# Optimization experiments

Measured on AMD Instinct MI355X. Metric: run time of the kernel, lower is better.

Reference implementation:

```python
import jax, jax.numpy as jnp
import numpy as np

ALPHA = 0.25
GAMMA = 2.0
MARGIN = 1.0
LAMBDA_GRAPH = 0.1
N = 8192
D = 128


def setup_inputs() -> dict:
    key = jax.random.key(0)
    k1, k2, k3, k4 = jax.random.split(key, 4)
    preds = jax.random.normal(k1, (N,), dtype=jnp.float32)
    targets = jax.random.randint(k2, (N,), 0, 2).astype(jnp.float32)  # binary labels
    features = jax.random.normal(k3, (N, D), dtype=jnp.float32)
    graph_features = jax.random.normal(k4, (N, D), dtype=jnp.float32)
    return {"preds": preds, "targets": targets, "features": features,
            "graph_features": graph_features}


def _focal_loss(preds, targets):
    # numerically stable BCE-with-logits, reduction='none'
    bce = jnp.maximum(preds, 0.0) - preds * targets + jnp.log1p(jnp.exp(-jnp.abs(preds)))
    pt = jnp.exp(-bce)
    return jnp.mean(ALPHA * (1.0 - pt) ** GAMMA * bce)


def _contrastive_loss(features, labels):
    # squared pairwise distances via ||a||^2 + ||b||^2 - 2 a.b  -> [N, N]
    sqn = jnp.sum(features * features, axis=-1)
    sq = sqn[:, None] + sqn[None, :] - 2.0 * (features @ features.T)
    sq = jnp.maximum(sq, 0.0)
    # safe sqrt (gradient-safe at 0)
    pos = sq > 0.0
    dist = jnp.where(pos, jnp.sqrt(jnp.where(pos, sq, 1.0)), 0.0)
    same = labels[:, None] == labels[None, :]
    # same-label pairs: dist^2 == sq ; different: clamp(margin - dist, 0)^2
    per_pair = jnp.where(same, sq, jnp.maximum(MARGIN - dist, 0.0) ** 2)
    return jnp.mean(per_pair)  # sum / N^2


def _graph_reg_loss(graph_features):
    diff = graph_features[1:] - graph_features[:-1]
    return jnp.mean(jnp.sqrt(jnp.sum(diff * diff, axis=1)))


def reference(preds, targets, features, graph_features):
    return (_focal_loss(preds, targets)
            + _contrastive_loss(features, targets)
            + LAMBDA_GRAPH * _graph_reg_loss(graph_features))
```

## Files before the change

### kernel.cpp

```cpp
#include <hip/hip_runtime.h>
#include <hip/hip_bf16.h>


#define N_PTS 8192
#define DIM 128

typedef __bf16 bf16x8 __attribute__((ext_vector_type(8)));
typedef float f32x4 __attribute__((ext_vector_type(4)));

#define FBF_OFF   0
#define SQN_OFF   (N_PTS * DIM * 2)
#define CPART_OFF (SQN_OFF + N_PTS * 4)
#define FPART_OFF (CPART_OFF + 4096 * 4)
#define GPART_OFF (FPART_OFF + 32 * 4)

__global__ __launch_bounds__(256) void prep_kernel(const float* __restrict__ feat,
                                                   __bf16* __restrict__ fbf,
                                                   float* __restrict__ sqn) {
    const int w = threadIdx.x >> 6;
    const int lane = threadIdx.x & 63;
    const int r = blockIdx.x * 4 + w;
    const float2 v = *reinterpret_cast<const float2*>(feat + r * DIM + lane * 2);
    union { __bf16 h[2]; unsigned u; } pk;
    pk.h[0] = (__bf16)v.x; pk.h[1] = (__bf16)v.y;
    reinterpret_cast<unsigned*>(fbf)[r * (DIM / 2) + lane] = pk.u;
    float s = v.x * v.x + v.y * v.y;
    #pragma unroll
    for (int off = 32; off > 0; off >>= 1) s += __shfl_down(s, off);
    if (lane == 0) sqn[r] = s;
}

__global__ __launch_bounds__(256) void focal_kernel(const float* __restrict__ preds,
                                                    const float* __restrict__ targets,
                                                    float* __restrict__ f_part) {
    const int i = blockIdx.x * 256 + threadIdx.x;
    const float p = preds[i], t = targets[i];
    const float bce = fmaxf(p, 0.f) - p * t + log1pf(expf(-fabsf(p)));
    const float pt = expf(-bce);
    const float om = 1.f - pt;
    float v = 0.25f * om * om * bce;
    #pragma unroll
    for (int off = 32; off > 0; off >>= 1) v += __shfl_down(v, off);
    __shared__ float red[4];
    if ((threadIdx.x & 63) == 0) red[threadIdx.x >> 6] = v;
    __syncthreads();
    if (threadIdx.x == 0) f_part[blockIdx.x] = red[0] + red[1] + red[2] + red[3];
}

__global__ __launch_bounds__(256) void graph_kernel(const float* __restrict__ gf,
                                                    float* __restrict__ g_part) {
    const int w = threadIdx.x >> 6;
    const int lane = threadIdx.x & 63;
    float acc = 0.f;
    #pragma unroll
    for (int it = 0; it < 8; ++it) {
        const int r = blockIdx.x * 4 + w + it * 1024;
        if (r < N_PTS - 1) {
            const float2 a = *reinterpret_cast<const float2*>(gf + r * DIM + lane * 2);
            const float2 b = *reinterpret_cast<const float2*>(gf + (r + 1) * DIM + lane * 2);
            const float dx = b.x - a.x, dy = b.y - a.y;
            float s = dx * dx + dy * dy;
            #pragma unroll
            for (int off = 32; off > 0; off >>= 1) s += __shfl_down(s, off);
            if (lane == 0) acc += sqrtf(s);
        }
    }
    __shared__ float red[4];
    if (lane == 0) red[w] = acc;
    __syncthreads();
    if (threadIdx.x == 0) g_part[blockIdx.x] = red[0] + red[1] + red[2] + red[3];
}

__global__ __launch_bounds__(256) void pair_kernel(const __bf16* __restrict__ fbf,
                                                   const float* __restrict__ sqn,
                                                   const float* __restrict__ targets,
                                                   float* __restrict__ c_part) {
    const int bi = blockIdx.x, bj = blockIdx.y;
    const int bid = bj * 64 + bi;
    if (bj < bi) {
        if (threadIdx.x == 0) c_part[bid] = 0.f;
        return;
    }
    __shared__ __align__(16) char smem[65536];
    const int tid = threadIdx.x;
    const int lane = tid & 63;
    const int wv = tid >> 6;
    const int quad = lane >> 4;
    const int m15 = lane & 15;
    const int ibase = bi * 128, jbase = bj * 128;

    #pragma unroll
    for (int it = 0; it < 16; ++it) {
        const int p = it * 256 + tid;
        const int r = (p & 2047) >> 4;
        const int s = p & 15;
        const int c = s ^ (r & 15);
        const int grow = ((p >> 11) ? jbase : ibase) + r;
        const uint4 v = *reinterpret_cast<const uint4*>(
            reinterpret_cast<const char*>(fbf) + grow * 256 + c * 16);
        *reinterpret_cast<uint4*>(smem + p * 16) = v;
    }
    __syncthreads();

    const int wm = wv >> 1, wn = wv & 1;
    f32x4 acc[4][4];
    #pragma unroll
    for (int a = 0; a < 4; ++a)
        #pragma unroll
        for (int b = 0; b < 4; ++b) acc[a][b] = (f32x4){0.f, 0.f, 0.f, 0.f};

    #pragma unroll
    for (int ks = 0; ks < 4; ++ks) {
        const int c = ks * 4 + quad;
        const int sw = (c ^ m15) << 4;
        bf16x8 af[4], bfv[4];
        #pragma unroll
        for (int t = 0; t < 4; ++t) {
            const int ra = wm * 64 + t * 16 + m15;
            const int rb = wn * 64 + t * 16 + m15;
            af[t]  = *reinterpret_cast<const bf16x8*>(smem + ra * 256 + sw);
            bfv[t] = *reinterpret_cast<const bf16x8*>(smem + 32768 + rb * 256 + sw);
        }
        #pragma unroll
        for (int tm = 0; tm < 4; ++tm)
            #pragma unroll
            for (int tn = 0; tn < 4; ++tn)
                acc[tm][tn] = __builtin_amdgcn_mfma_f32_16x16x32_bf16(
                    af[tm], bfv[tn], acc[tm][tn], 0, 0, 0);
    }

    const bool diag = (bi == bj);
    float lsum = 0.f;
    #pragma unroll
    for (int tm = 0; tm < 4; ++tm) {
        const int i0 = wm * 64 + tm * 16 + quad * 4;
        const f32x4 sqni = *reinterpret_cast<const f32x4*>(sqn + ibase + i0);
        const f32x4 ti   = *reinterpret_cast<const f32x4*>(targets + ibase + i0);
        #pragma unroll
        for (int tn = 0; tn < 4; ++tn) {
            const int jl = wn * 64 + tn * 16 + m15;
            const float sqnj = sqn[jbase + jl];
            const float tj = targets[jbase + jl];
            #pragma unroll
            for (int e = 0; e < 4; ++e) {
                const float g = acc[tm][tn][e];
                const float sq = fmaxf(sqni[e] + sqnj - 2.f * g, 0.f);
                const float d = sqrtf(sq);
                const float m = fmaxf(1.f - d, 0.f);
                const float v = (ti[e] == tj) ? sq : m * m;
                float w;
                if (!diag) {
                    w = 2.f;
                } else {
                    const int il = i0 + e;
                    w = (jl > il) ? 2.f : ((jl == il) ? 1.f : 0.f);
                }
                lsum += w * v;
            }
        }
    }
    #pragma unroll
    for (int off = 32; off > 0; off >>= 1) lsum += __shfl_down(lsum, off);
    __syncthreads();
    float* red = reinterpret_cast<float*>(smem);
    if (lane == 0) red[wv] = lsum;
    __syncthreads();
    if (tid == 0) c_part[bid] = red[0] + red[1] + red[2] + red[3];
}

__global__ __launch_bounds__(256) void finalize_kernel(const float* __restrict__ c_part,
                                                       const float* __restrict__ f_part,
                                                       const float* __restrict__ g_part,
                                                       float* __restrict__ out) {
    const int tid = threadIdx.x;
    float c = 0.f;
    for (int i = tid; i < 4096; i += 256) c += c_part[i];
    float f = (tid < 32) ? f_part[tid] : 0.f;
    float g = g_part[tid];
    #pragma unroll
    for (int off = 32; off > 0; off >>= 1) {
        c += __shfl_down(c, off);
        f += __shfl_down(f, off);
        g += __shfl_down(g, off);
    }
    __shared__ float red[12];
    const int w = tid >> 6, lane = tid & 63;
    if (lane == 0) { red[w] = c; red[4 + w] = f; red[8 + w] = g; }
    __syncthreads();
    if (tid == 0) {
        const float cs = red[0] + red[1] + red[2] + red[3];
        const float fs = red[4] + red[5] + red[6] + red[7];
        const float gs = red[8] + red[9] + red[10] + red[11];
        out[0] = cs / (8192.f * 8192.f) + fs / 8192.f + 0.1f * (gs / 8191.f);
    }
}

extern "C" void kernel_launch(void* const* d_in, const int* in_sizes, int n_in,
                              void* d_out, int out_size, void* d_ws, size_t ws_size,
                              hipStream_t stream) {
    const float* preds    = (const float*)d_in[0];
    const float* targets  = (const float*)d_in[1];
    const float* features = (const float*)d_in[2];
    const float* gfeat    = (const float*)d_in[3];
    char* ws = (char*)d_ws;
    __bf16* fbf   = (__bf16*)(ws + FBF_OFF);
    float* sqn    = (float*)(ws + SQN_OFF);
    float* c_part = (float*)(ws + CPART_OFF);
    float* f_part = (float*)(ws + FPART_OFF);
    float* g_part = (float*)(ws + GPART_OFF);
    float* out = (float*)d_out;

    prep_kernel<<<2048, 256, 0, stream>>>(features, fbf, sqn);
    focal_kernel<<<32, 256, 0, stream>>>(preds, targets, f_part);
    graph_kernel<<<256, 256, 0, stream>>>(gfeat, g_part);
    pair_kernel<<<dim3(64, 64), 256, 0, stream>>>(fbf, sqn, targets, c_part);
    finalize_kernel<<<1, 256, 0, stream>>>(c_part, f_part, g_part, out);
}
```

Measured before the change: 127.6 us.

## Compute same-label pair sum in closed form and skip far-apart different-label pairs

The same-label squared-distance sum is now computed algebraically from per-class feature sums and norms (n*sum||x||^2 - ||sum x||^2), so the pair kernel only handles different-label pairs. Each wave first takes the minimum squared distance over its tile and runs the sqrt/margin path only when some pair falls inside the margin. The pair grid is launched as only the 2080 upper-triangle tiles, and operands load straight from global into registers without the LDS staging. The prep, focal and graph kernels merge into one launch. The closed form depends on float sums of large terms (partly combined in double), which risks cancellation error.

After: 128.3 us. Within noise of the previous version (+0.6%).

```diff
diff --git a/kernel.cpp b/kernel.cpp
--- a/kernel.cpp
+++ b/kernel.cpp
@@ -11,98 +11,171 @@
 #define FBF_OFF   0
 #define SQN_OFF   (N_PTS * DIM * 2)
 #define CPART_OFF (SQN_OFF + N_PTS * 4)
-#define FPART_OFF (CPART_OFF + 4096 * 4)
+#define FPART_OFF (CPART_OFF + 8320 * 4)
 #define GPART_OFF (FPART_OFF + 32 * 4)
-
-__global__ __launch_bounds__(256) void prep_kernel(const float* __restrict__ feat,
-                                                   __bf16* __restrict__ fbf,
-                                                   float* __restrict__ sqn) {
-    const int w = threadIdx.x >> 6;
-    const int lane = threadIdx.x & 63;
-    const int r = blockIdx.x * 4 + w;
-    const float2 v = *reinterpret_cast<const float2*>(feat + r * DIM + lane * 2);
-    union { __bf16 h[2]; unsigned u; } pk;
-    pk.h[0] = (__bf16)v.x; pk.h[1] = (__bf16)v.y;
-    reinterpret_cast<unsigned*>(fbf)[r * (DIM / 2) + lane] = pk.u;
-    float s = v.x * v.x + v.y * v.y;
-    #pragma unroll
-    for (int off = 32; off > 0; off >>= 1) s += __shfl_down(s, off);
-    if (lane == 0) sqn[r] = s;
-}
-
-__global__ __launch_bounds__(256) void focal_kernel(const float* __restrict__ preds,
-                                                    const float* __restrict__ targets,
-                                                    float* __restrict__ f_part) {
-    const int i = blockIdx.x * 256 + threadIdx.x;
-    const float p = preds[i], t = targets[i];
-    const float bce = fmaxf(p, 0.f) - p * t + log1pf(expf(-fabsf(p)));
-    const float pt = expf(-bce);
-    const float om = 1.f - pt;
-    float v = 0.25f * om * om * bce;
-    #pragma unroll
-    for (int off = 32; off > 0; off >>= 1) v += __shfl_down(v, off);
-    __shared__ float red[4];
-    if ((threadIdx.x & 63) == 0) red[threadIdx.x >> 6] = v;
-    __syncthreads();
-    if (threadIdx.x == 0) f_part[blockIdx.x] = red[0] + red[1] + red[2] + red[3];
-}
-
-__global__ __launch_bounds__(256) void graph_kernel(const float* __restrict__ gf,
-                                                    float* __restrict__ g_part) {
-    const int w = threadIdx.x >> 6;
-    const int lane = threadIdx.x & 63;
-    float acc = 0.f;
-    #pragma unroll
-    for (int it = 0; it < 8; ++it) {
-        const int r = blockIdx.x * 4 + w + it * 1024;
-        if (r < N_PTS - 1) {
-            const float2 a = *reinterpret_cast<const float2*>(gf + r * DIM + lane * 2);
-            const float2 b = *reinterpret_cast<const float2*>(gf + (r + 1) * DIM + lane * 2);
-            const float dx = b.x - a.x, dy = b.y - a.y;
-            float s = dx * dx + dy * dy;
+#define VPART_OFF (GPART_OFF + 256 * 4)
+
+__global__ __launch_bounds__(256) void aux_kernel(const float* __restrict__ feat,
+                                                  const float* __restrict__ preds,
+                                                  const float* __restrict__ targets,
+                                                  const float* __restrict__ gfeat,
+                                                  __bf16* __restrict__ fbf,
+                                                  float* __restrict__ sqn,
+                                                  float* __restrict__ vpart,
+                                                  float* __restrict__ f_part,
+                                                  float* __restrict__ g_part) {
+    __shared__ float smem[1024];
+    const int bx = blockIdx.x;
+    const int tid = threadIdx.x;
+    const int w = tid >> 6;
+    const int lane = tid & 63;
+
+    if (bx < 128) {
+        float sx = 0.f, sy = 0.f, c1x = 0.f, c1y = 0.f;
+        #pragma unroll
+        for (int it = 0; it < 16; ++it) {
+            const int r = bx * 64 + it * 4 + w;
+            const float2 v = *reinterpret_cast<const float2*>(feat + r * DIM + lane * 2);
+            const float t = targets[r];
+            union { __bf16 h[2]; unsigned u; } pk;
+            pk.h[0] = (__bf16)v.x; pk.h[1] = (__bf16)v.y;
+            reinterpret_cast<unsigned*>(fbf)[r * (DIM / 2) + lane] = pk.u;
+            float s = v.x * v.x + v.y * v.y;
             #pragma unroll
             for (int off = 32; off > 0; off >>= 1) s += __shfl_down(s, off);
-            if (lane == 0) acc += sqrtf(s);
-        }
-    }
-    __shared__ float red[4];
-    if (lane == 0) red[w] = acc;
-    __syncthreads();
-    if (threadIdx.x == 0) g_part[blockIdx.x] = red[0] + red[1] + red[2] + red[3];
-}
-
-__global__ __launch_bounds__(256) void pair_kernel(const __bf16* __restrict__ fbf,
-                                                   const float* __restrict__ sqn,
-                                                   const float* __restrict__ targets,
-                                                   float* __restrict__ c_part) {
-    const int bi = blockIdx.x, bj = blockIdx.y;
-    const int bid = bj * 64 + bi;
-    if (bj < bi) {
-        if (threadIdx.x == 0) c_part[bid] = 0.f;
-        return;
-    }
-    __shared__ __align__(16) char smem[65536];
+            if (lane == 0) sqn[r] = s;
+            sx += v.x; sy += v.y;
+            c1x += t * v.x; c1y += t * v.y;
+        }
+        smem[w * 256 + 2 * lane]       = sx - c1x;
+        smem[w * 256 + 2 * lane + 1]   = sy - c1y;
+        smem[w * 256 + 128 + 2 * lane]     = c1x;
+        smem[w * 256 + 128 + 2 * lane + 1] = c1y;
+        __syncthreads();
+        vpart[bx * 256 + tid] = smem[tid] + smem[256 + tid] + smem[512 + tid] + smem[768 + tid];
+    } else if (bx < 160) {
+        const int b = bx - 128;
+        const int i = b * 256 + tid;
+        const float p = preds[i], t = targets[i];
+        const float bce = fmaxf(p, 0.f) - p * t + log1pf(expf(-fabsf(p)));
+        const float pt = expf(-bce);
+        const float om = 1.f - pt;
+        float v = 0.25f * om * om * bce;
+        #pragma unroll
+        for (int off = 32; off > 0; off >>= 1) v += __shfl_down(v, off);
+        if (lane == 0) smem[w] = v;
+        __syncthreads();
+        if (tid == 0) f_part[b] = smem[0] + smem[1] + smem[2] + smem[3];
+    } else {
+        const int b = bx - 160;
+        float acc = 0.f;
+        #pragma unroll
+        for (int it = 0; it < 8; ++it) {
+            const int r = b * 4 + w + it * 1024;
+            if (r < N_PTS - 1) {
+                const float2 a = *reinterpret_cast<const float2*>(gfeat + r * DIM + lane * 2);
+                const float2 bb = *reinterpret_cast<const float2*>(gfeat + (r + 1) * DIM + lane * 2);
+                const float dx = bb.x - a.x, dy = bb.y - a.y;
+                float s = dx * dx + dy * dy;
+                #pragma unroll
+                for (int off = 32; off > 0; off >>= 1) s += __shfl_down(s, off);
+                if (lane == 0) acc += sqrtf(s);
+            }
+        }
+        if (lane == 0) smem[w] = acc;
+        __syncthreads();
+        if (tid == 0) g_part[b] = smem[0] + smem[1] + smem[2] + smem[3];
+    }
+}
+
+template<bool DIAG>
+__device__ __forceinline__ float scan_min(const f32x4 (&acc)[4][4],
+                                          const f32x4 (&sqni)[4], const f32x4 (&ti4)[4],
+                                          const float (&sqnj)[4], const float (&tj4)[4],
+                                          int wm, int wn, int quad, int m15) {
+    float minkey = 1e30f;
+    #pragma unroll
+    for (int tm = 0; tm < 4; ++tm) {
+        #pragma unroll
+        for (int tn = 0; tn < 4; ++tn) {
+            const int jl = wn * 64 + tn * 16 + m15;
+            #pragma unroll
+            for (int e = 0; e < 4; ++e) {
+                const float sq = sqni[tm][e] + sqnj[tn] - 2.f * acc[tm][tn][e];
+                bool excl = (ti4[tm][e] == tj4[tn]);
+                if (DIAG) {
+                    const int il = wm * 64 + tm * 16 + quad * 4 + e;
+                    excl = excl || (jl <= il);
+                }
+                minkey = fminf(minkey, excl ? 1e30f : sq);
+            }
+        }
+    }
+    return minkey;
+}
+
+template<bool DIAG>
+__device__ __forceinline__ float scan_slow(const f32x4 (&acc)[4][4],
+                                           const f32x4 (&sqni)[4], const f32x4 (&ti4)[4],
+                                           const float (&sqnj)[4], const float (&tj4)[4],
+                                           int wm, int wn, int quad, int m15) {
+    float lsum = 0.f;
+    #pragma unroll
+    for (int tm = 0; tm < 4; ++tm) {
+        #pragma unroll
+        for (int tn = 0; tn < 4; ++tn) {
+            const int jl = wn * 64 + tn * 16 + m15;
+            #pragma unroll
+            for (int e = 0; e < 4; ++e) {
+                const float sq = sqni[tm][e] + sqnj[tn] - 2.f * acc[tm][tn][e];
+                bool excl = (ti4[tm][e] == tj4[tn]);
+                if (DIAG) {
+                    const int il = wm * 64 + tm * 16 + quad * 4 + e;
+                    excl = excl || (jl <= il);
+                }
+                if (!excl && sq < 1.f) {
+                    const float d = sqrtf(fmaxf(sq, 0.f));
+                    const float m = 1.f - d;
+                    lsum += 2.f * m * m;
+                }
+            }
+        }
+    }
+    return lsum;
+}
+
+__global__ __launch_bounds__(256, 2) void pair_kernel(const __bf16* __restrict__ fbf,
+                                                      const float* __restrict__ sqn,
+                                                      const float* __restrict__ targets,
+                                                      float* __restrict__ c_part) {
+    const int u = blockIdx.x;
+    const int v = 2079 - u;
+    int k = (int)((sqrtf(8.f * (float)v + 1.f) - 1.f) * 0.5f);
+    while ((k + 1) * (k + 2) / 2 <= v) ++k;
+    while (k * (k + 1) / 2 > v) --k;
+    const int bi = 63 - k;
+    const int bj = 63 - (v - k * (k + 1) / 2);
+
     const int tid = threadIdx.x;
     const int lane = tid & 63;
     const int wv = tid >> 6;
     const int quad = lane >> 4;
     const int m15 = lane & 15;
+    const int wm = wv >> 1, wn = wv & 1;
     const int ibase = bi * 128, jbase = bj * 128;
 
-    #pragma unroll
-    for (int it = 0; it < 16; ++it) {
-        const int p = it * 256 + tid;
-        const int r = (p & 2047) >> 4;
-        const int s = p & 15;
-        const int c = s ^ (r & 15);
-        const int grow = ((p >> 11) ? jbase : ibase) + r;
-        const uint4 v = *reinterpret_cast<const uint4*>(
-            reinterpret_cast<const char*>(fbf) + grow * 256 + c * 16);
-        *reinterpret_cast<uint4*>(smem + p * 16) = v;
-    }
-    __syncthreads();
-
-    const int wm = wv >> 1, wn = wv & 1;
+    const char* fb = reinterpret_cast<const char*>(fbf);
+    const char* arow = fb + (size_t)(ibase + wm * 64 + m15) * 256 + quad * 16;
+    const char* brow = fb + (size_t)(jbase + wn * 64 + m15) * 256 + quad * 16;
+    bf16x8 af[4][4], bfr[4][4];
+    #pragma unroll
+    for (int t = 0; t < 4; ++t)
+        #pragma unroll
+        for (int ks = 0; ks < 4; ++ks) {
+            af[t][ks]  = *reinterpret_cast<const bf16x8*>(arow + t * 4096 + ks * 64);
+            bfr[t][ks] = *reinterpret_cast<const bf16x8*>(brow + t * 4096 + ks * 64);
+        }
+
     f32x4 acc[4][4];
     #pragma unroll
     for (int a = 0; a < 4; ++a)
@@ -110,88 +183,104 @@
         for (int b = 0; b < 4; ++b) acc[a][b] = (f32x4){0.f, 0.f, 0.f, 0.f};
 
     #pragma unroll
-    for (int ks = 0; ks < 4; ++ks) {
-        const int c = ks * 4 + quad;
-        const int sw = (c ^ m15) << 4;
-        bf16x8 af[4], bfv[4];
-        #pragma unroll
-        for (int t = 0; t < 4; ++t) {
-            const int ra = wm * 64 + t * 16 + m15;
-            const int rb = wn * 64 + t * 16 + m15;
-            af[t]  = *reinterpret_cast<const bf16x8*>(smem + ra * 256 + sw);
-            bfv[t] = *reinterpret_cast<const bf16x8*>(smem + 32768 + rb * 256 + sw);
-        }
+    for (int ks = 0; ks < 4; ++ks)
         #pragma unroll
         for (int tm = 0; tm < 4; ++tm)
             #pragma unroll
             for (int tn = 0; tn < 4; ++tn)
                 acc[tm][tn] = __builtin_amdgcn_mfma_f32_16x16x32_bf16(
-                    af[tm], bfv[tn], acc[tm][tn], 0, 0, 0);
-    }
-
-    const bool diag = (bi == bj);
-    float lsum = 0.f;
+                    af[tm][ks], bfr[tn][ks], acc[tm][tn], 0, 0, 0);
+
+    f32x4 sqni[4], ti4[4];
+    float sqnj[4], tj4[4];
     #pragma unroll
     for (int tm = 0; tm < 4; ++tm) {
         const int i0 = wm * 64 + tm * 16 + quad * 4;
-        const f32x4 sqni = *reinterpret_cast<const f32x4*>(sqn + ibase + i0);
-        const f32x4 ti   = *reinterpret_cast<const f32x4*>(targets + ibase + i0);
-        #pragma unroll
-        for (int tn = 0; tn < 4; ++tn) {
-            const int jl = wn * 64 + tn * 16 + m15;
-            const float sqnj = sqn[jbase + jl];
-            const float tj = targets[jbase + jl];
-            #pragma unroll
-            for (int e = 0; e < 4; ++e) {
-                const float g = acc[tm][tn][e];
-                const float sq = fmaxf(sqni[e] + sqnj - 2.f * g, 0.f);
-                const float d = sqrtf(sq);
-                const float m = fmaxf(1.f - d, 0.f);
-                const float v = (ti[e] == tj) ? sq : m * m;
-                float w;
-                if (!diag) {
-                    w = 2.f;
-                } else {
-                    const int il = i0 + e;
-                    w = (jl > il) ? 2.f : ((jl == il) ? 1.f : 0.f);
-                }
-                lsum += w * v;
-            }
-        }
-    }
-    #pragma unroll
-    for (int off = 32; off > 0; off >>= 1) lsum += __shfl_down(lsum, off);
-    __syncthreads();
-    float* red = reinterpret_cast<float*>(smem);
-    if (lane == 0) red[wv] = lsum;
-    __syncthreads();
-    if (tid == 0) c_part[bid] = red[0] + red[1] + red[2] + red[3];
+        sqni[tm] = *reinterpret_cast<const f32x4*>(sqn + ibase + i0);
+        ti4[tm]  = *reinterpret_cast<const f32x4*>(targets + ibase + i0);
+    }
+    #pragma unroll
+    for (int tn = 0; tn < 4; ++tn) {
+        const int jl = wn * 64 + tn * 16 + m15;
+        sqnj[tn] = sqn[jbase + jl];
+        tj4[tn]  = targets[jbase + jl];
+    }
+
+    const bool diag = (bi == bj);
+    const float minkey = diag
+        ? scan_min<true >(acc, sqni, ti4, sqnj, tj4, wm, wn, quad, m15)
+        : scan_min<false>(acc, sqni, ti4, sqnj, tj4, wm, wn, quad, m15);
+
+    float lsum = 0.f;
+    if (minkey < 1.f)
+        lsum = diag
+            ? scan_slow<true >(acc, sqni, ti4, sqnj, tj4, wm, wn, quad, m15)
+            : scan_slow<false>(acc, sqni, ti4, sqnj, tj4, wm, wn, quad, m15);
+
+    float wsum = 0.f;
+    if (__any(minkey < 1.f)) {
+        #pragma unroll
+        for (int off = 32; off > 0; off >>= 1) lsum += __shfl_down(lsum, off);
+        wsum = lsum;
+    }
+    if (lane == 0) c_part[u * 4 + wv] = wsum;
 }
 
 __global__ __launch_bounds__(256) void finalize_kernel(const float* __restrict__ c_part,
                                                        const float* __restrict__ f_part,
                                                        const float* __restrict__ g_part,
+                                                       const float* __restrict__ vpart,
+                                                       const float* __restrict__ sqn,
+                                                       const float* __restrict__ targets,
                                                        float* __restrict__ out) {
+    __shared__ float red[32];
     const int tid = threadIdx.x;
+    const int w = tid >> 6, lane = tid & 63;
+
     float c = 0.f;
-    for (int i = tid; i < 4096; i += 256) c += c_part[i];
+    for (int i = tid; i < 8320; i += 256) c += c_part[i];
     float f = (tid < 32) ? f_part[tid] : 0.f;
     float g = g_part[tid];
+
+    float V = 0.f;
+    for (int b = 0; b < 128; ++b) V += vpart[b * 256 + tid];
+    float vsq = V * V;
+
+    float stot = 0.f, s1 = 0.f, n1 = 0.f;
+    for (int i = tid; i < N_PTS; i += 256) {
+        const float s = sqn[i], t = targets[i];
+        stot += s; s1 += t * s; n1 += t;
+    }
+
     #pragma unroll
     for (int off = 32; off > 0; off >>= 1) {
         c += __shfl_down(c, off);
         f += __shfl_down(f, off);
         g += __shfl_down(g, off);
-    }
-    __shared__ float red[12];
-    const int w = tid >> 6, lane = tid & 63;
-    if (lane == 0) { red[w] = c; red[4 + w] = f; red[8 + w] = g; }
+        vsq  += __shfl_down(vsq, off);
+        stot += __shfl_down(stot, off);
+        s1   += __shfl_down(s1, off);
+        n1   += __shfl_down(n1, off);
+    }
+    if (lane == 0) {
+        red[w] = c; red[4 + w] = f; red[8 + w] = g;
+        red[12 + w] = vsq; red[16 + w] = stot; red[20 + w] = s1; red[24 + w] = n1;
+    }
     __syncthreads();
     if (tid == 0) {
-        const float cs = red[0] + red[1] + red[2] + red[3];
-        const float fs = red[4] + red[5] + red[6] + red[7];
-        const float gs = red[8] + red[9] + red[10] + red[11];
-        out[0] = cs / (8192.f * 8192.f) + fs / 8192.f + 0.1f * (gs / 8191.f);
+        const double cs = (double)red[0] + red[1] + red[2] + red[3];
+        const double fs = (double)red[4] + red[5] + red[6] + red[7];
+        const double gs = (double)red[8] + red[9] + red[10] + red[11];
+        const double v0sq = (double)red[12] + red[13];
+        const double v1sq = (double)red[14] + red[15];
+        const double st = (double)red[16] + red[17] + red[18] + red[19];
+        const double s1s = (double)red[20] + red[21] + red[22] + red[23];
+        const double n1s = (double)red[24] + red[25] + red[26] + red[27];
+        const double n0s = (double)N_PTS - n1s;
+        const double s0s = st - s1s;
+        const double same = 2.0 * (n0s * s0s - v0sq) + 2.0 * (n1s * s1s - v1sq);
+        out[0] = (float)((cs + same) / ((double)N_PTS * N_PTS)
+                         + fs / N_PTS + 0.1 * (gs / (N_PTS - 1)));
     }
 }
 
@@ -208,11 +297,11 @@
     float* c_part = (float*)(ws + CPART_OFF);
     float* f_part = (float*)(ws + FPART_OFF);
     float* g_part = (float*)(ws + GPART_OFF);
+    float* vpart  = (float*)(ws + VPART_OFF);
     float* out = (float*)d_out;
 
-    prep_kernel<<<2048, 256, 0, stream>>>(features, fbf, sqn);
-    focal_kernel<<<32, 256, 0, stream>>>(preds, targets, f_part);
-    graph_kernel<<<256, 256, 0, stream>>>(gfeat, g_part);
-    pair_kernel<<<dim3(64, 64), 256, 0, stream>>>(fbf, sqn, targets, c_part);
-    finalize_kernel<<<1, 256, 0, stream>>>(c_part, f_part, g_part, out);
-}
+    aux_kernel<<<416, 256, 0, stream>>>(features, preds, targets, gfeat,
+                                        fbf, sqn, vpart, f_part, g_part);
+    pair_kernel<<<2080, 256, 0, stream>>>(fbf, sqn, targets, c_part);
+    finalize_kernel<<<1, 256, 0, stream>>>(c_part, f_part, g_part, vpart, sqn, targets, out);
+}
```
